# Optimization experiments

Measured on AMD Instinct MI355X. Metric: run time of the kernel, lower is better.

## Reference

```python
import jax, jax.numpy as jnp
import numpy as np

IN_F = 4096
OUT_F = 4096
NNZ = int(0.01 * IN_F * OUT_F)
ALPHA = 1.0


def setup_inputs() -> dict:
    key = jax.random.key(0)
    k1, k2, k3, k4, k5 = jax.random.split(key, 5)
    x = jax.random.normal(k1, (4, 2048, IN_F), dtype=jnp.float32)
    base_weights = (jax.random.normal(k2, (OUT_F, IN_F), dtype=jnp.float32) * 0.02).astype(jnp.float16)
    # sparse outlier correction in COO form (equivalent content to the CSR buffers)
    ortho_vals = (jax.random.normal(k3, (NNZ,), dtype=jnp.float32) * 1e-3).astype(jnp.float16)
    ortho_rows = jax.random.randint(k4, (NNZ,), 0, OUT_F, dtype=jnp.int32)
    ortho_cols = jax.random.randint(k5, (NNZ,), 0, IN_F, dtype=jnp.int32)
    return {"x": x, "base_weights": base_weights, "ortho_vals": ortho_vals,
            "ortho_rows": ortho_rows, "ortho_cols": ortho_cols}


def reference(x, base_weights, ortho_vals, ortho_rows, ortho_cols):
    orig_shape = x.shape
    orig_dtype = x.dtype
    x_flat = x.reshape(-1, IN_F)  # [N, in]

    # Base stream: fp16 GEMM, then cast to fp32 (matches torch.mm on fp16)
    out_base = jnp.matmul(x_flat.astype(jnp.float16), base_weights.T).astype(jnp.float32)

    # Ortho stream: sparse (out,in) correction applied in fp32.
    # Scatter the sparse values into a dense fp32 matrix once (cheap: 64MB),
    # then use a dense GEMM — same math as torch.sparse.mm(W_csr, x^T)^T.
    w_ortho = jnp.zeros((OUT_F, IN_F), dtype=jnp.float32).at[ortho_rows, ortho_cols].add(
        ortho_vals.astype(jnp.float32))
    out_ortho = jnp.matmul(x_flat.astype(jnp.float32), w_ortho.T)  # [N, out]

    out_flat = out_base + ALPHA * out_ortho
    return out_flat.reshape(orig_shape[:-1] + (OUT_F,)).astype(orig_dtype)
```

## Files before the change

kernel.cpp:

```cpp
#include <hip/hip_runtime.h>

typedef _Float16 f16;
typedef unsigned short u16;
typedef unsigned int u32;
typedef long long i64;
typedef __attribute__((ext_vector_type(8))) _Float16 f16x8;
typedef __attribute__((ext_vector_type(4))) float f32x4;

#define IN_F 4096
#define OUT_F 4096

__device__ __forceinline__ void gload16(const f16* g, f16* l) {
  __builtin_amdgcn_global_load_lds(
      (const __attribute__((address_space(1))) void*)g,
      (__attribute__((address_space(3))) void*)l, 16, 0, 0);
}

__global__ __launch_bounds__(256) void cvt_f32_f16(
    const float* __restrict__ in, f16* __restrict__ out, i64 n8) {
  i64 s = (i64)gridDim.x * blockDim.x;
  for (i64 j = (i64)blockIdx.x * blockDim.x + threadIdx.x; j < n8; j += s) {
    float4 a = ((const float4*)in)[2 * j];
    float4 b = ((const float4*)in)[2 * j + 1];
    f16x8 o;
    o[0] = (f16)a.x; o[1] = (f16)a.y; o[2] = (f16)a.z; o[3] = (f16)a.w;
    o[4] = (f16)b.x; o[5] = (f16)b.y; o[6] = (f16)b.z; o[7] = (f16)b.w;
    ((f16x8*)out)[j] = o;
  }
}

__global__ __launch_bounds__(256) void zero32(u32* __restrict__ p, i64 n) {
  i64 s = (i64)gridDim.x * blockDim.x;
  for (i64 j = (i64)blockIdx.x * blockDim.x + threadIdx.x; j < n; j += s) p[j] = 0u;
}

__global__ __launch_bounds__(256) void scatter_woh(
    const float* __restrict__ vals, const int* __restrict__ rows,
    const int* __restrict__ cols, f16* __restrict__ woh, int nnz) {
  int i = blockIdx.x * blockDim.x + threadIdx.x;
  if (i >= nnz) return;
  int r = rows[i], c = cols[i];
  if (r < 0 || r >= OUT_F || c < 0 || c >= IN_F) return;
  float v = vals[i];
  size_t idx = (size_t)r * IN_F + c;
  u32* p = (u32*)woh + (idx >> 1);
  u32 sh = (u32)(idx & 1) * 16u;
  union { f16 h; u16 u; } cv;
  u32 old = *p;
  while (true) {
    u32 assumed = old;
    cv.u = (u16)((assumed >> sh) & 0xFFFFu);
    float cur = (float)cv.h;
    cv.h = (f16)(cur + v);
    u32 nw = (assumed & ~(0xFFFFu << sh)) | ((u32)cv.u << sh);
    old = atomicCAS(p, assumed, nw);
    if (old == assumed) break;
  }
}

template <int STREAM>
__global__ __launch_bounds__(512, 2) void gemm_256(
    const f16* __restrict__ Xh, const f16* __restrict__ Bm,
    float* __restrict__ out, int M) {
  __shared__ alignas(16) f16 As[2][16384];
  __shared__ alignas(16) f16 Bs[2][16384];

  const int tid = threadIdx.x;
  const int lane = tid & 63;
  const int wave = tid >> 6;
  const int wr = wave >> 2;
  const int wc = wave & 3;
  const int lo = lane & 15, hi = lane >> 4, l7 = lane & 7;

  const int bid = (int)blockIdx.x;
  const int nbn = OUT_F / 256;
  const int nwg = (M / 256) * nbn;
  const int swz = ((nwg & 7) == 0) ? ((bid & 7) * (nwg >> 3) + (bid >> 3)) : bid;
  const int brow = (swz / nbn) << 8;
  const int bcol = (swz % nbn) << 8;

  int aglob[4], bglob[4], ldst[4];
#pragma unroll
  for (int i = 0; i < 4; ++i) {
    int c = i * 512 + tid;
    int row = c >> 3;
    int kc = (c & 7) ^ (row & 7);
    ldst[i] = c * 8;
    aglob[i] = (brow + row) * IN_F + kc * 8;
    bglob[i] = (bcol + row) * IN_F + kc * 8;
  }

  const int abase = (wr * 128 + lo) * 64;
  const int bbase = (wc * 64 + lo) * 64;
  const int slot0 = ((hi) ^ l7) * 8;
  const int slot1 = ((4 + hi) ^ l7) * 8;

  f32x4 acc[8][4] = {};

#pragma unroll
  for (int i = 0; i < 4; ++i) {
    gload16(Xh + aglob[i], &As[0][ldst[i]]);
    gload16(Bm + bglob[i], &Bs[0][ldst[i]]);
  }
#pragma unroll
  for (int i = 0; i < 4; ++i) {
    gload16(Xh + aglob[i] + 64, &As[1][ldst[i]]);
    gload16(Bm + bglob[i] + 64, &Bs[1][ldst[i]]);
  }
  asm volatile("s_waitcnt vmcnt(8)" ::: "memory");
  __builtin_amdgcn_sched_barrier(0);
  __builtin_amdgcn_s_barrier();

  const int NT = IN_F / 64;
  for (int kt = 0; kt < NT; ++kt) {
    const f16* A = As[kt & 1];
    const f16* B = Bs[kt & 1];

    f16x8 bf[4][2];
#pragma unroll
    for (int nf = 0; nf < 4; ++nf) {
      bf[nf][0] = *(const f16x8*)(B + bbase + nf * 1024 + slot0);
      bf[nf][1] = *(const f16x8*)(B + bbase + nf * 1024 + slot1);
    }
#pragma unroll
    for (int q = 0; q < 4; ++q) {
      f16x8 a00 = *(const f16x8*)(A + abase + (2 * q)     * 1024 + slot0);
      f16x8 a01 = *(const f16x8*)(A + abase + (2 * q)     * 1024 + slot1);
      f16x8 a10 = *(const f16x8*)(A + abase + (2 * q + 1) * 1024 + slot0);
      f16x8 a11 = *(const f16x8*)(A + abase + (2 * q + 1) * 1024 + slot1);
      __builtin_amdgcn_s_setprio(1);
#pragma unroll
      for (int nf = 0; nf < 4; ++nf) {
        acc[2 * q][nf]     = __builtin_amdgcn_mfma_f32_16x16x32_f16(a00, bf[nf][0], acc[2 * q][nf], 0, 0, 0);
        acc[2 * q][nf]     = __builtin_amdgcn_mfma_f32_16x16x32_f16(a01, bf[nf][1], acc[2 * q][nf], 0, 0, 0);
        acc[2 * q + 1][nf] = __builtin_amdgcn_mfma_f32_16x16x32_f16(a10, bf[nf][0], acc[2 * q + 1][nf], 0, 0, 0);
        acc[2 * q + 1][nf] = __builtin_amdgcn_mfma_f32_16x16x32_f16(a11, bf[nf][1], acc[2 * q + 1][nf], 0, 0, 0);
      }
      __builtin_amdgcn_s_setprio(0);
    }

    __builtin_amdgcn_s_barrier();
    if (kt + 2 < NT) {
      f16* An = (f16*)As[kt & 1];
      f16* Bn = (f16*)Bs[kt & 1];
      const int kn = (kt + 2) * 64;
#pragma unroll
      for (int i = 0; i < 4; ++i) {
        gload16(Xh + aglob[i] + kn, An + ldst[i]);
        gload16(Bm + bglob[i] + kn, Bn + ldst[i]);
      }
    }
    if (kt + 1 < NT) {
      if (kt + 2 < NT) asm volatile("s_waitcnt vmcnt(8)" ::: "memory");
      else             asm volatile("s_waitcnt vmcnt(0)" ::: "memory");
      __builtin_amdgcn_sched_barrier(0);
      __builtin_amdgcn_s_barrier();
    }
  }

  const int crow0 = brow + wr * 128 + (hi << 2);
  const int ccol0 = bcol + wc * 64 + lo;
#pragma unroll
  for (int mf = 0; mf < 8; ++mf)
#pragma unroll
    for (int nf = 0; nf < 4; ++nf)
#pragma unroll
      for (int r = 0; r < 4; ++r) {
        float* p = out + (size_t)(crow0 + mf * 16 + r) * OUT_F + (ccol0 + nf * 16);
        if constexpr (STREAM == 0)
          *p = (float)(f16)acc[mf][nf][r];
        else
          *p += acc[mf][nf][r];
      }
}

template <bool A16, int STREAM>
__global__ __launch_bounds__(256, 2) void gemm_one(
    const float* __restrict__ Xf, const f16* __restrict__ Xh,
    const f16* __restrict__ Bm, float* __restrict__ out, int M) {
  constexpr int LDA = A16 ? 32 : 40;
  __shared__ alignas(16) f16 As[128 * LDA];
  __shared__ alignas(16) f16 Bs[128 * 32];

  const int tid = threadIdx.x, lane = tid & 63, wave = tid >> 6;
  const int wr = wave >> 1, wc = wave & 1;
  const int nbn = OUT_F / 128;
  const int nwg = (int)gridDim.x;
  const int bid = (int)blockIdx.x;
  const int swz = ((nwg & 7) == 0) ? ((bid & 7) * (nwg >> 3) + (bid >> 3)) : bid;
  const int brow = (swz / nbn) << 7;
  const int bcol = (swz % nbn) << 7;

  f32x4 acc[4][4] = {};
  const int srow = tid >> 2, sk = (tid & 3) * 8;
  const f16* gB = Bm + (size_t)(bcol + srow) * IN_F + sk;
  f16* sB = Bs + tid * 8;
  const f16*   gA = A16 ? (Xh + (size_t)(brow + srow) * IN_F + sk) : (const f16*)nullptr;
  const float* gX = A16 ? (const float*)nullptr : (Xf + (size_t)(brow + srow) * IN_F + sk);
  f16* sA  = As + tid * 8;
  f16* sAr = As + srow * LDA + sk;
  const f16* pa = As + (wr * 64 + (lane & 15)) * LDA + (lane >> 4) * 8;
  const f16* pb = Bs + (wc * 64 + (lane & 15)) * 32 + (lane >> 4) * 8;

  for (int k0 = 0; k0 < IN_F; k0 += 32) {
    if constexpr (A16) {
      gload16(gA + k0, sA);
      gload16(gA + k0 + (size_t)64 * IN_F, sA + 2048);
    } else {
      float4 u0 = *(const float4*)(gX + k0);
      float4 u1 = *(const float4*)(gX + k0 + 4);
      float4 v0 = *(const float4*)(gX + k0 + (size_t)64 * IN_F);
      float4 v1 = *(const float4*)(gX + k0 + (size_t)64 * IN_F + 4);
      f16x8 h0, h1;
      h0[0] = (f16)u0.x; h0[1] = (f16)u0.y; h0[2] = (f16)u0.z; h0[3] = (f16)u0.w;
      h0[4] = (f16)u1.x; h0[5] = (f16)u1.y; h0[6] = (f16)u1.z; h0[7] = (f16)u1.w;
      h1[0] = (f16)v0.x; h1[1] = (f16)v0.y; h1[2] = (f16)v0.z; h1[3] = (f16)v0.w;
      h1[4] = (f16)v1.x; h1[5] = (f16)v1.y; h1[6] = (f16)v1.z; h1[7] = (f16)v1.w;
      *(f16x8*)sAr = h0;
      *(f16x8*)(sAr + 64 * LDA) = h1;
    }
    gload16(gB + k0, sB);
    gload16(gB + k0 + (size_t)64 * IN_F, sB + 2048);
    __syncthreads();
    f16x8 af[4], bfr[4];
#pragma unroll
    for (int m = 0; m < 4; ++m) af[m] = *(const f16x8*)(pa + m * 16 * LDA);
#pragma unroll
    for (int n = 0; n < 4; ++n) bfr[n] = *(const f16x8*)(pb + n * 512);
#pragma unroll
    for (int m = 0; m < 4; ++m)
#pragma unroll
      for (int n = 0; n < 4; ++n)
        acc[m][n] = __builtin_amdgcn_mfma_f32_16x16x32_f16(af[m], bfr[n], acc[m][n], 0, 0, 0);
    __syncthreads();
  }
  const int crow0 = brow + wr * 64 + ((lane >> 4) << 2);
  const int ccol0 = bcol + wc * 64 + (lane & 15);
#pragma unroll
  for (int m = 0; m < 4; ++m)
#pragma unroll
    for (int n = 0; n < 4; ++n)
#pragma unroll
      for (int r = 0; r < 4; ++r) {
        float* p = out + (size_t)(crow0 + m * 16 + r) * OUT_F + (ccol0 + n * 16);
        if constexpr (STREAM == 0) *p = (float)(f16)acc[m][n][r];
        else *p += acc[m][n][r];
      }
}

extern "C" void kernel_launch(void* const* d_in, const int* in_sizes, int n_in,
                              void* d_out, int out_size, void* d_ws, size_t ws_size,
                              hipStream_t stream) {
  const float* x    = (const float*)d_in[0];
  const float* W    = (const float*)d_in[1];
  const float* vals = (const float*)d_in[2];
  const int*   rows = (const int*)d_in[3];
  const int*   cols = (const int*)d_in[4];
  float*       out  = (float*)d_out;

  const i64 total_x = (i64)in_sizes[0];
  const int M   = (int)(total_x / IN_F);
  const int nnz = in_sizes[2];
  if (M <= 0 || M % 128 != 0) return;

  const size_t whb = (size_t)OUT_F * IN_F * 2;
  const size_t xhb = (size_t)M * IN_F * 2;

  if (ws_size >= xhb + 2 * whb) {
    f16* xh  = (f16*)d_ws;
    f16* wh  = (f16*)((char*)d_ws + xhb);
    f16* woh = (f16*)((char*)d_ws + xhb + whb);
    cvt_f32_f16<<<2048, 256, 0, stream>>>(x, xh, total_x / 8);
    cvt_f32_f16<<<2048, 256, 0, stream>>>(W, wh, (i64)OUT_F * IN_F / 8);
    zero32<<<2048, 256, 0, stream>>>((u32*)woh, (i64)(whb / 4));
    scatter_woh<<<(nnz + 255) / 256, 256, 0, stream>>>(vals, rows, cols, woh, nnz);
    if (M % 256 == 0) {
      const int grid = (M / 256) * (OUT_F / 256);
      gemm_256<0><<<grid, 512, 0, stream>>>(xh, wh, out, M);
      gemm_256<1><<<grid, 512, 0, stream>>>(xh, woh, out, M);
    } else {
      const int grid = (M / 128) * (OUT_F / 128);
      gemm_one<true, 0><<<grid, 256, 0, stream>>>(nullptr, xh, wh, out, M);
      gemm_one<true, 1><<<grid, 256, 0, stream>>>(nullptr, xh, woh, out, M);
    }
  } else if (ws_size >= 2 * whb) {
    f16* wh  = (f16*)d_ws;
    f16* woh = (f16*)((char*)d_ws + whb);
    cvt_f32_f16<<<2048, 256, 0, stream>>>(W, wh, (i64)OUT_F * IN_F / 8);
    zero32<<<2048, 256, 0, stream>>>((u32*)woh, (i64)(whb / 4));
    scatter_woh<<<(nnz + 255) / 256, 256, 0, stream>>>(vals, rows, cols, woh, nnz);
    const int grid = (M / 128) * (OUT_F / 128);
    gemm_one<false, 0><<<grid, 256, 0, stream>>>(x, nullptr, wh, out, M);
    gemm_one<false, 1><<<grid, 256, 0, stream>>>(x, nullptr, woh, out, M);
  }
}
```

Measured before the change: 623.0 us.

## Interleave LDS fragment reads and global prefetch with MFMA steps; XCD-aware tile mapping

Restructures the GEMM main loop into seven software-pipelined steps. Each step loads the next A fragment from LDS and issues part of the next tile's global-to-LDS prefetch while MFMAs run on the current fragment. Prefetch distance drops from two tiles ahead to one, with a single barrier per k-tile. It also adds an explicit block-to-tile mapping for the 32x16 tile grid so that each XCD works on an 8x8 patch, to improve L2 reuse. The risks are less memory latency hiding, since it now waits on vmcnt(0) every iteration, and a leftover dead load that reads the B buffer from a computed offset off As.

```diff
diff --git a/kernel.cpp b/kernel.cpp
--- a/kernel.cpp
+++ b/kernel.cpp
@@ -74,10 +74,22 @@
 
   const int bid = (int)blockIdx.x;
   const int nbn = OUT_F / 256;
-  const int nwg = (M / 256) * nbn;
-  const int swz = ((nwg & 7) == 0) ? ((bid & 7) * (nwg >> 3) + (bid >> 3)) : bid;
-  const int brow = (swz / nbn) << 8;
-  const int bcol = (swz % nbn) << 8;
+  const int nbm = M / 256;
+  int browi, bcoli;
+  if (nbm == 32 && nbn == 16) {
+    const int xcd = bid & 7;
+    const int j   = bid >> 3;
+    const int jr  = j >> 3, jc = j & 7;
+    browi = (xcd & 3) * 8 + jr;
+    bcoli = (xcd >> 2) * 8 + jc;
+  } else {
+    const int nwg = nbm * nbn;
+    const int swz = ((nwg & 7) == 0) ? ((bid & 7) * (nwg >> 3) + (bid >> 3)) : bid;
+    browi = swz / nbn;
+    bcoli = swz % nbn;
+  }
+  const int brow = browi << 8;
+  const int bcol = bcoli << 8;
 
   int aglob[4], bglob[4], ldst[4];
 #pragma unroll
@@ -96,67 +108,104 @@
   const int slot1 = ((4 + hi) ^ l7) * 8;
 
   f32x4 acc[8][4] = {};
-
-#pragma unroll
-  for (int i = 0; i < 4; ++i) {
-    gload16(Xh + aglob[i], &As[0][ldst[i]]);
-    gload16(Bm + bglob[i], &Bs[0][ldst[i]]);
-  }
-#pragma unroll
-  for (int i = 0; i < 4; ++i) {
-    gload16(Xh + aglob[i] + 64, &As[1][ldst[i]]);
-    gload16(Bm + bglob[i] + 64, &Bs[1][ldst[i]]);
-  }
+  f16x8 bf[4][2], afA[2], afB[2];
+
+  gload16(Bm + bglob[0], &Bs[0][ldst[0]]);
+  gload16(Bm + bglob[1], &Bs[0][ldst[1]]);
+  gload16(Bm + bglob[2], &Bs[0][ldst[2]]);
+  gload16(Bm + bglob[3], &Bs[0][ldst[3]]);
+  gload16(Xh + aglob[0], &As[0][ldst[0]]);
+  gload16(Xh + aglob[1], &As[0][ldst[1]]);
+  gload16(Xh + aglob[2], &As[0][ldst[2]]);
+  gload16(Xh + aglob[3], &As[0][ldst[3]]);
+  gload16(Bm + bglob[0] + 64, &Bs[1][ldst[0]]);
+  gload16(Bm + bglob[1] + 64, &Bs[1][ldst[1]]);
+  gload16(Bm + bglob[2] + 64, &Bs[1][ldst[2]]);
+  gload16(Bm + bglob[3] + 64, &Bs[1][ldst[3]]);
+  gload16(Xh + aglob[0] + 64, &As[1][ldst[0]]);
+  gload16(Xh + aglob[1] + 64, &As[1][ldst[1]]);
+  gload16(Xh + aglob[2] + 64, &As[1][ldst[2]]);
+  gload16(Xh + aglob[3] + 64, &As[1][ldst[3]]);
   asm volatile("s_waitcnt vmcnt(8)" ::: "memory");
   __builtin_amdgcn_sched_barrier(0);
   __builtin_amdgcn_s_barrier();
 
+#pragma unroll
+  for (int nf = 0; nf < 4; ++nf) {
+    bf[nf][0] = *(const f16x8*)(&As[0][0] + 16384 * 2 + bbase + nf * 1024 + slot0);
+  }
+#pragma unroll
+  for (int nf = 0; nf < 4; ++nf) {
+    bf[nf][0] = *(const f16x8*)(&Bs[0][bbase + nf * 1024 + slot0]);
+    bf[nf][1] = *(const f16x8*)(&Bs[0][bbase + nf * 1024 + slot1]);
+  }
+  afA[0] = *(const f16x8*)(&As[0][abase + 0 * 1024 + slot0]);
+  afA[1] = *(const f16x8*)(&As[0][abase + 0 * 1024 + slot1]);
+
+#define STEP(RD, RDIDX, MM, MMIDX, STG)                                       \
+  RD[0] = *(const f16x8*)(A + abase + (RDIDX) * 1024 + slot0);                \
+  RD[1] = *(const f16x8*)(A + abase + (RDIDX) * 1024 + slot1);                \
+  STG;                                                                         \
+  __builtin_amdgcn_sched_barrier(0);                                           \
+  __builtin_amdgcn_s_setprio(1);                                               \
+  _Pragma("unroll")                                                            \
+  for (int ks = 0; ks < 2; ++ks)                                               \
+    _Pragma("unroll")                                                          \
+    for (int nf = 0; nf < 4; ++nf)                                             \
+      acc[MMIDX][nf] = __builtin_amdgcn_mfma_f32_16x16x32_f16(                 \
+          MM[ks], bf[nf][ks], acc[MMIDX][nf], 0, 0, 0);                        \
+  __builtin_amdgcn_s_setprio(0);                                               \
+  __builtin_amdgcn_sched_barrier(0);
+
   const int NT = IN_F / 64;
   for (int kt = 0; kt < NT; ++kt) {
-    const f16* A = As[kt & 1];
-    const f16* B = Bs[kt & 1];
-
-    f16x8 bf[4][2];
-#pragma unroll
-    for (int nf = 0; nf < 4; ++nf) {
-      bf[nf][0] = *(const f16x8*)(B + bbase + nf * 1024 + slot0);
-      bf[nf][1] = *(const f16x8*)(B + bbase + nf * 1024 + slot1);
+    const f16* A = &As[kt & 1][0];
+    f16* An = &As[(kt & 1) ^ 1][0];
+    f16* Bn = &Bs[(kt & 1) ^ 1][0];
+    const int kn = (kt + 1) * 64;
+    const bool pf = (kt + 1 < NT);
+
+    STEP(afB, 1, afA, 0, if (pf) { gload16(Bm + bglob[0] + kn, Bn + ldst[0]);
+                                   gload16(Bm + bglob[1] + kn, Bn + ldst[1]); })
+    STEP(afA, 2, afB, 1, if (pf) { gload16(Bm + bglob[2] + kn, Bn + ldst[2]);
+                                   gload16(Bm + bglob[3] + kn, Bn + ldst[3]); })
+    STEP(afB, 3, afA, 2, if (pf) { gload16(Xh + aglob[0] + kn, An + ldst[0]);
+                                   gload16(Xh + aglob[2] + kn, An + ldst[2]); })
+    STEP(afA, 4, afB, 3, if (pf) { gload16(Xh + aglob[1] + kn, An + ldst[1]);
+                                   gload16(Xh + aglob[3] + kn, An + ldst[3]); })
+    STEP(afB, 5, afA, 4, (void)0)
+    STEP(afA, 6, afB, 5, (void)0)
+    STEP(afB, 7, afA, 6, (void)0)
+
+    asm volatile("s_waitcnt lgkmcnt(0)" ::: "memory");
+    __builtin_amdgcn_sched_barrier(0);
+    asm volatile("s_waitcnt vmcnt(0)" ::: "memory");
+    __builtin_amdgcn_sched_barrier(0);
+    __builtin_amdgcn_s_barrier();
+
+    __builtin_amdgcn_s_setprio(1);
+#pragma unroll
+    for (int ks = 0; ks < 2; ++ks)
+#pragma unroll
+      for (int nf = 0; nf < 4; ++nf)
+        acc[7][nf] = __builtin_amdgcn_mfma_f32_16x16x32_f16(
+            afB[ks], bf[nf][ks], acc[7][nf], 0, 0, 0);
+    __builtin_amdgcn_s_setprio(0);
+    __builtin_amdgcn_sched_barrier(0);
+
+    if (pf) {
+      const f16* A2 = &As[(kt & 1) ^ 1][0];
+      const f16* B2 = &Bs[(kt & 1) ^ 1][0];
+#pragma unroll
+      for (int nf = 0; nf < 4; ++nf) {
+        bf[nf][0] = *(const f16x8*)(B2 + bbase + nf * 1024 + slot0);
+        bf[nf][1] = *(const f16x8*)(B2 + bbase + nf * 1024 + slot1);
+      }
+      afA[0] = *(const f16x8*)(A2 + abase + 0 * 1024 + slot0);
+      afA[1] = *(const f16x8*)(A2 + abase + 0 * 1024 + slot1);
     }
-#pragma unroll
-    for (int q = 0; q < 4; ++q) {
-      f16x8 a00 = *(const f16x8*)(A + abase + (2 * q)     * 1024 + slot0);
-      f16x8 a01 = *(const f16x8*)(A + abase + (2 * q)     * 1024 + slot1);
-      f16x8 a10 = *(const f16x8*)(A + abase + (2 * q + 1) * 1024 + slot0);
-      f16x8 a11 = *(const f16x8*)(A + abase + (2 * q + 1) * 1024 + slot1);
-      __builtin_amdgcn_s_setprio(1);
-#pragma unroll
-      for (int nf = 0; nf < 4; ++nf) {
-        acc[2 * q][nf]     = __builtin_amdgcn_mfma_f32_16x16x32_f16(a00, bf[nf][0], acc[2 * q][nf], 0, 0, 0);
-        acc[2 * q][nf]     = __builtin_amdgcn_mfma_f32_16x16x32_f16(a01, bf[nf][1], acc[2 * q][nf], 0, 0, 0);
-        acc[2 * q + 1][nf] = __builtin_amdgcn_mfma_f32_16x16x32_f16(a10, bf[nf][0], acc[2 * q + 1][nf], 0, 0, 0);
-        acc[2 * q + 1][nf] = __builtin_amdgcn_mfma_f32_16x16x32_f16(a11, bf[nf][1], acc[2 * q + 1][nf], 0, 0, 0);
-      }
-      __builtin_amdgcn_s_setprio(0);
-    }
-
-    __builtin_amdgcn_s_barrier();
-    if (kt + 2 < NT) {
-      f16* An = (f16*)As[kt & 1];
-      f16* Bn = (f16*)Bs[kt & 1];
-      const int kn = (kt + 2) * 64;
-#pragma unroll
-      for (int i = 0; i < 4; ++i) {
-        gload16(Xh + aglob[i] + kn, An + ldst[i]);
-        gload16(Bm + bglob[i] + kn, Bn + ldst[i]);
-      }
-    }
-    if (kt + 1 < NT) {
-      if (kt + 2 < NT) asm volatile("s_waitcnt vmcnt(8)" ::: "memory");
-      else             asm volatile("s_waitcnt vmcnt(0)" ::: "memory");
-      __builtin_amdgcn_sched_barrier(0);
-      __builtin_amdgcn_s_barrier();
-    }
-  }
+  }
+#undef STEP
 
   const int crow0 = brow + wr * 128 + (hi << 2);
   const int ccol0 = bcol + wc * 64 + lo;
```

Result: faster. 587.6 us (-5.7%).
